# Performance work log

Measured on AMD Instinct MI355X. Metric: run time of the kernel, lower is better.

The kernel has to match this reference:

```python
import jax, jax.numpy as jnp
import numpy as np

GH, GW, H, B, IN = 4, 2, 512, 8192, 1
FC_HID = H // 2
NC = GH * GW
BN_EPS = 1e-5


def setup_inputs() -> dict:
    key = jax.random.key(0)
    ks = jax.random.split(key, 20)
    def n(k, shape, s=1.0):
        return jax.random.normal(k, shape, dtype=jnp.float32) * s
    return {
        "x": n(ks[0], (B, GH, GW)),
        "h_ext": n(ks[1], (B, H), 0.1),
        "c_ext": n(ks[2], (B, H), 0.1),
        "grid_h": n(ks[3], (GH, GW, B, H), 0.1),
        "grid_c": n(ks[4], (GH, GW, B, H), 0.1),
        "Wh": n(ks[5], (NC, H, 3 * H), (3 * H) ** -0.5),
        "bh": n(ks[6], (NC, H), 0.01),
        "Wc": n(ks[7], (NC, H, 3 * H), (3 * H) ** -0.5),
        "bc": n(ks[8], (NC, H), 0.01),
        "W_ih": n(ks[9], (NC, 4 * H, IN), 1.0),
        "W_hh": n(ks[10], (NC, 4 * H, H), H ** -0.5),
        "b_ih": n(ks[11], (NC, 4 * H), 0.01),
        "b_hh": n(ks[12], (NC, 4 * H), 0.01),
        "W1": n(ks[13], (FC_HID, 2 * H), (2 * H) ** -0.5),
        "b1": n(ks[14], (FC_HID,), 0.01),
        "W2": n(ks[15], (1, FC_HID), FC_HID ** -0.5),
        "b2": n(ks[16], (1,), 0.01),
        "gamma": jnp.ones((1,), jnp.float32),
        "beta": jnp.zeros((1,), jnp.float32),
    }


def _lattice_forward(x, h_ext, c_ext, grid_h, grid_c, Wh, bh, Wc, bc,
                     W_ih, W_hh, b_ih, b_hh, W1, b1, W2, b2, gamma, beta):
    b = x.shape[0]
    zeros = jnp.zeros((b, H), x.dtype)
    # python lists over the small fixed 4x2 grid (strict left/up dependency)
    sh = [[grid_h[i, j] for j in range(GW)] for i in range(GH)]
    sc = [[grid_c[i, j] for j in range(GW)] for i in range(GH)]
    for i in range(GH):
        for j in range(GW):
            k = i * GW + j
            h_prev, c_prev = sh[i][j], sc[i][j]
            if i == 0 and j == 0:
                h_left, c_left = h_ext, c_ext
            elif j > 0:
                h_left, c_left = sh[i][j - 1], sc[i][j - 1]
            else:
                h_left, c_left = zeros, zeros
            if i > 0:
                h_up, c_up = sh[i - 1][j], sc[i - 1][j]
            else:
                h_up, c_up = zeros, zeros
            comb_h = jnp.concatenate([h_left, h_up, h_prev], axis=1)  # [B,3H]
            comb_c = jnp.concatenate([c_left, c_up, c_prev], axis=1)
            ph = comb_h @ Wh[k].T + bh[k]  # [B,H]
            pc = comb_c @ Wc[k].T + bc[k]
            xi = x[:, i, j][:, None]  # [B,1]
            gates = xi @ W_ih[k].T + b_ih[k] + ph @ W_hh[k].T + b_hh[k]  # [B,4H]
            ig, fg, gg, og = jnp.split(gates, 4, axis=1)
            c_new = jax.nn.sigmoid(fg) * pc + jax.nn.sigmoid(ig) * jnp.tanh(gg)
            h_new = jax.nn.sigmoid(og) * jnp.tanh(c_new)
            sh[i][j], sc[i][j] = h_new, c_new
    final_h = sh[-1][-1] + h_ext
    final_c = sc[-1][-1] + c_ext
    final = jnp.concatenate([final_h, final_c], axis=1)  # [B,2H]
    hid = jax.nn.relu(final @ W1.T + b1)
    out = hid @ W2.T + b2  # [B,1]
    # BatchNorm1d in training mode: biased batch stats over the batch dim
    mu = jnp.mean(out, axis=0, keepdims=True)
    var = jnp.mean((out - mu) ** 2, axis=0, keepdims=True)
    out = gamma * (out - mu) * jax.lax.rsqrt(var + BN_EPS) + beta
    out = jax.nn.sigmoid(out)
    new_gh = jnp.stack([jnp.stack(row) for row in sh])  # [GH,GW,B,H]
    new_gc = jnp.stack([jnp.stack(row) for row in sc])
    return out, final_h, final_c, new_gh, new_gc


def reference(x, h_ext, c_ext, grid_h, grid_c, Wh, bh, Wc, bc,
              W_ih, W_hh, b_ih, b_hh, W1, b1, W2, b2, gamma, beta):
    return _lattice_forward(x, h_ext, c_ext, grid_h, grid_c, Wh, bh, Wc, bc,
                            W_ih, W_hh, b_ih, b_hh, W1, b1, W2, b2, gamma, beta)
```

## Files before the change

### kernel.cpp

```cpp
#include <hip/hip_runtime.h>
#include <stdint.h>

#define B_SZ 8192
#define H_SZ 512
static const size_t BH = (size_t)B_SZ * H_SZ;

typedef short bfrag8 __attribute__((ext_vector_type(8)));
typedef float f32x4 __attribute__((ext_vector_type(4)));

__device__ __forceinline__ unsigned short f2bf(float f) {
  union { float f; uint32_t u; } c; c.f = f;
  uint32_t u = c.u;
  uint32_t r = (u + 0x7FFFu + ((u >> 16) & 1u)) >> 16;
  return (unsigned short)r;
}
__device__ __forceinline__ float bf2f(unsigned short u) {
  union { uint32_t u; float f; } c; c.u = ((uint32_t)u) << 16;
  return c.f;
}
__device__ __forceinline__ float sigm(float x) { return 1.0f / (1.0f + __expf(-x)); }
__device__ __forceinline__ float tanh_fast(float x) {
  float cx = fminf(fmaxf(x, -15.0f), 15.0f);
  float e = __expf(2.0f * cx);
  return (e - 1.0f) / (e + 1.0f);
}

__device__ __forceinline__ void gload16(const void* g, void* l) {
  __builtin_amdgcn_global_load_lds(
      (const __attribute__((address_space(1))) void*)g,
      (__attribute__((address_space(3))) void*)l, 16, 0, 0);
}

__device__ __forceinline__ void xcd_swizzle(int& bx, int& by, int& bz) {
  int nx = gridDim.x, ny = gridDim.y, nz = gridDim.z;
  int nwg = nx * ny * nz;
  int id = blockIdx.x + nx * (blockIdx.y + ny * blockIdx.z);
  int q = nwg >> 3, r = nwg & 7;
  int xcd = id & 7, lin = id >> 3;
  int swz = (xcd < r ? xcd * (q + 1) : r * (q + 1) + (xcd - r) * q) + lin;
  bx = swz % nx; swz /= nx;
  by = swz % ny; bz = swz / ny;
}

struct PJob {
  const unsigned short* A[3];
  int co[3];
  int nseg, relu;
  const unsigned short* B;
  const float* bias;
  unsigned short* outBf;
  float* outF;
};
struct PArgs {
  PJob j[8];
  int ldA, ldB, outStride;
};

__global__ __launch_bounds__(256, 4) void pgemm_k(PArgs pa) {
  __shared__ __align__(16) char As[16384];
  __shared__ __align__(16) char Bs[16384];
  int bx, by, bz;
  xcd_swizzle(bx, by, bz);
  const PJob jb = pa.j[bz];
  const int tid = threadIdx.x;
  const int lane = tid & 63;
  const int wv = tid >> 6;
  const int wr = wv >> 1, wc = wv & 1;
  const int m0 = by * 128;

  int rowA[4], cg[4];
  const char* browPtr[4];
#pragma unroll
  for (int q = 0; q < 4; ++q) {
    int cl = q * 256 + tid;
    int row = cl >> 3, cs = cl & 7;
    cg[q] = cs ^ (row & 7);
    rowA[q] = row;
    browPtr[q] = (const char*)jb.B + (size_t)(bx * 128 + row) * pa.ldB * 2;
  }

  f32x4 acc[4][4];
#pragma unroll
  for (int a = 0; a < 4; ++a)
#pragma unroll
    for (int b = 0; b < 4; ++b) acc[a][b] = f32x4{0.f, 0.f, 0.f, 0.f};

  for (int s = 0; s < jb.nseg; ++s) {
    const char* Abase = (const char*)jb.A[s];
    const int coB = jb.co[s] * 2;
    for (int k0 = 0; k0 < 512; k0 += 64) {
#pragma unroll
      for (int q = 0; q < 4; ++q)
        gload16(Abase + ((size_t)(m0 + rowA[q]) * pa.ldA + k0) * 2 + cg[q] * 16,
                As + (q * 256 + tid) * 16);
#pragma unroll
      for (int q = 0; q < 4; ++q)
        gload16(browPtr[q] + coB + k0 * 2 + cg[q] * 16,
                Bs + (q * 256 + tid) * 16);
      __syncthreads();
#pragma unroll
      for (int ks = 0; ks < 2; ++ks) {
        bfrag8 af[4], bfr[4];
#pragma unroll
        for (int mf = 0; mf < 4; ++mf) {
          int row = wr * 64 + mf * 16 + (lane & 15);
          af[mf] = *(const bfrag8*)(As + row * 128 +
                                    ((ks * 4 + (lane >> 4)) ^ (row & 7)) * 16);
        }
#pragma unroll
        for (int nf = 0; nf < 4; ++nf) {
          int row = wc * 64 + nf * 16 + (lane & 15);
          bfr[nf] = *(const bfrag8*)(Bs + row * 128 +
                                     ((ks * 4 + (lane >> 4)) ^ (row & 7)) * 16);
        }
#pragma unroll
        for (int mf = 0; mf < 4; ++mf)
#pragma unroll
          for (int nf = 0; nf < 4; ++nf)
            acc[mf][nf] = __builtin_amdgcn_mfma_f32_16x16x32_bf16(
                af[mf], bfr[nf], acc[mf][nf], 0, 0, 0);
      }
      __syncthreads();
    }
  }

  const int c4 = lane & 15;
  const int r4 = lane >> 4;
  const int n0 = bx * 128;
#pragma unroll
  for (int nf = 0; nf < 4; ++nf) {
    int colg = n0 + wc * 64 + nf * 16 + c4;
    float bv = jb.bias[colg];
#pragma unroll
    for (int mf = 0; mf < 4; ++mf)
#pragma unroll
      for (int r = 0; r < 4; ++r) {
        int rowg = m0 + wr * 64 + mf * 16 + r4 * 4 + r;
        size_t o = (size_t)rowg * pa.outStride + colg;
        float v = acc[mf][nf][r] + bv;
        if (jb.relu) v = fmaxf(v, 0.0f);
        if (jb.outBf) jb.outBf[o] = f2bf(v);
        if (jb.outF) jb.outF[o] = v;
      }
  }
}

struct GJob {
  const unsigned short* ph;
  const unsigned short* Whh;
  const float* pc;
  float* gh; float* gc;
  unsigned short* nh; unsigned short* nc;
  int cell, last;
};
struct GArgs {
  GJob j[2];
  const float* x;
  const float* W_ih; const float* b_ih; const float* b_hh;
  const float* h_ext; const float* c_ext;
  float* fh; float* fc;
  unsigned short* finalB;
};

__global__ __launch_bounds__(256, 3) void gates_k(GArgs ga) {
  __shared__ __align__(16) char As[16384];
  __shared__ __align__(16) char Bs[16384];
  int bx, by, bz;
  xcd_swizzle(bx, by, bz);
  const GJob jb = ga.j[bz];
  const int tid = threadIdx.x;
  const int lane = tid & 63;
  const int wv = tid >> 6;
  const int wr = wv >> 1, wc = wv & 1;
  const int m0 = by * 128;

  int rowA[4], cg[4];
  const char* browPtr[4];
#pragma unroll
  for (int q = 0; q < 4; ++q) {
    int cl = q * 256 + tid;
    int row = cl >> 3, cs = cl & 7;
    cg[q] = cs ^ (row & 7);
    rowA[q] = row;
    int gate = (row >> 4) & 3;
    int hh = bx * 32 + ((row >> 6) << 4) + (row & 15);
    browPtr[q] = (const char*)jb.Whh + (size_t)(gate * 512 + hh) * 512 * 2;
  }

  f32x4 acc[4][4];
#pragma unroll
  for (int a = 0; a < 4; ++a)
#pragma unroll
    for (int b = 0; b < 4; ++b) acc[a][b] = f32x4{0.f, 0.f, 0.f, 0.f};

  for (int k0 = 0; k0 < 512; k0 += 64) {
#pragma unroll
    for (int q = 0; q < 4; ++q)
      gload16((const char*)jb.ph + ((size_t)(m0 + rowA[q]) * 512 + k0) * 2 + cg[q] * 16,
              As + (q * 256 + tid) * 16);
#pragma unroll
    for (int q = 0; q < 4; ++q)
      gload16(browPtr[q] + k0 * 2 + cg[q] * 16, Bs + (q * 256 + tid) * 16);
    __syncthreads();
#pragma unroll
    for (int ks = 0; ks < 2; ++ks) {
      bfrag8 af[4], bfr[4];
#pragma unroll
      for (int mf = 0; mf < 4; ++mf) {
        int row = wr * 64 + mf * 16 + (lane & 15);
        af[mf] = *(const bfrag8*)(As + row * 128 +
                                  ((ks * 4 + (lane >> 4)) ^ (row & 7)) * 16);
      }
#pragma unroll
      for (int nf = 0; nf < 4; ++nf) {
        int row = wc * 64 + nf * 16 + (lane & 15);
        bfr[nf] = *(const bfrag8*)(Bs + row * 128 +
                                   ((ks * 4 + (lane >> 4)) ^ (row & 7)) * 16);
      }
#pragma unroll
      for (int mf = 0; mf < 4; ++mf)
#pragma unroll
        for (int nf = 0; nf < 4; ++nf)
          acc[mf][nf] = __builtin_amdgcn_mfma_f32_16x16x32_bf16(
              af[mf], bfr[nf], acc[mf][nf], 0, 0, 0);
    }
    __syncthreads();
  }

  const int c4 = lane & 15;
  const int r4 = lane >> 4;
  int hcol = bx * 32 + wc * 16 + c4;
  const float* Wih = ga.W_ih + jb.cell * 2048;
  const float* bih = ga.b_ih + jb.cell * 2048;
  const float* bhh = ga.b_hh + jb.cell * 2048;
  float wih[4], gb[4];
#pragma unroll
  for (int q = 0; q < 4; ++q) {
    wih[q] = Wih[q * 512 + hcol];
    gb[q] = bih[q * 512 + hcol] + bhh[q * 512 + hcol];
  }
#pragma unroll
  for (int mf = 0; mf < 4; ++mf)
#pragma unroll
    for (int r = 0; r < 4; ++r) {
      int b = m0 + wr * 64 + mf * 16 + r4 * 4 + r;
      float xi = ga.x[b * 8 + jb.cell];
      float vi = acc[mf][0][r] + xi * wih[0] + gb[0];
      float vf = acc[mf][1][r] + xi * wih[1] + gb[1];
      float vg = acc[mf][2][r] + xi * wih[2] + gb[2];
      float vo = acc[mf][3][r] + xi * wih[3] + gb[3];
      size_t o = (size_t)b * 512 + hcol;
      float pcv = jb.pc[o];
      float cn = sigm(vf) * pcv + sigm(vi) * tanh_fast(vg);
      float hn = sigm(vo) * tanh_fast(cn);
      jb.gh[o] = hn;
      jb.gc[o] = cn;
      jb.nh[o] = f2bf(hn);
      jb.nc[o] = f2bf(cn);
      if (jb.last) {
        float fh = hn + ga.h_ext[o];
        float fc = cn + ga.c_ext[o];
        ga.fh[o] = fh;
        ga.fc[o] = fc;
        ga.finalB[(size_t)b * 1024 + hcol] = f2bf(fh);
        ga.finalB[(size_t)b * 1024 + 512 + hcol] = f2bf(fc);
      }
    }
}

struct CvtArgs {
  const float4* s[8];
  uint2* d[8];
  long start[9];
};
__global__ __launch_bounds__(256) void convert_many(CvtArgs ca) {
  long total = ca.start[8];
  long stride = (long)gridDim.x * blockDim.x;
  for (long idx = (long)blockIdx.x * blockDim.x + threadIdx.x; idx < total;
       idx += stride) {
    int jb = 0;
#pragma unroll
    for (int q = 1; q < 8; ++q) jb += (idx >= ca.start[q]) ? 1 : 0;
    long local = idx - ca.start[jb];
    float4 v = ca.s[jb][local];
    uint2 o;
    o.x = (uint32_t)f2bf(v.x) | ((uint32_t)f2bf(v.y) << 16);
    o.y = (uint32_t)f2bf(v.z) | ((uint32_t)f2bf(v.w) << 16);
    ca.d[jb][local] = o;
  }
}

__global__ __launch_bounds__(256)
void fc2_kernel(const unsigned short* hid, const float* W2, const float* b2,
                float* outlin) {
  int row = blockIdx.x * 4 + (threadIdx.x >> 6);
  int lane = threadIdx.x & 63;
  uint2 hv = ((const uint2*)(hid + (size_t)row * 256))[lane];
  float4 wv = ((const float4*)W2)[lane];
  float s = bf2f((unsigned short)(hv.x & 0xffffu)) * wv.x +
            bf2f((unsigned short)(hv.x >> 16)) * wv.y +
            bf2f((unsigned short)(hv.y & 0xffffu)) * wv.z +
            bf2f((unsigned short)(hv.y >> 16)) * wv.w;
#pragma unroll
  for (int o = 32; o > 0; o >>= 1) s += __shfl_down(s, o);
  if (lane == 0) outlin[row] = s + b2[0];
}

__global__ __launch_bounds__(1024)
void bn_kernel(const float* outlin, const float* gamma, const float* beta,
               float* out) {
  __shared__ float sred[16], sred2[16];
  __shared__ float smu, srs;
  float s = 0.f, s2 = 0.f;
  for (int i = threadIdx.x; i < 8192; i += 1024) {
    float v = outlin[i];
    s += v; s2 += v * v;
  }
#pragma unroll
  for (int o = 32; o > 0; o >>= 1) { s += __shfl_down(s, o); s2 += __shfl_down(s2, o); }
  if ((threadIdx.x & 63) == 0) { sred[threadIdx.x >> 6] = s; sred2[threadIdx.x >> 6] = s2; }
  __syncthreads();
  if (threadIdx.x == 0) {
    float S = 0.f, S2 = 0.f;
    for (int q = 0; q < 16; ++q) { S += sred[q]; S2 += sred2[q]; }
    float mu = S * (1.0f / 8192.0f);
    float var = S2 * (1.0f / 8192.0f) - mu * mu;
    smu = mu; srs = rsqrtf(var + 1e-5f);
  }
  __syncthreads();
  float gm = gamma[0], bt = beta[0];
  for (int i = threadIdx.x; i < 8192; i += 1024) {
    float v = (outlin[i] - smu) * srs * gm + bt;
    out[i] = sigm(v);
  }
}

extern "C" void kernel_launch(void* const* d_in, const int* in_sizes, int n_in,
                              void* d_out, int out_size, void* d_ws, size_t ws_size,
                              hipStream_t stream) {
  const float* x      = (const float*)d_in[0];
  const float* h_ext  = (const float*)d_in[1];
  const float* c_ext  = (const float*)d_in[2];
  const float* grid_h = (const float*)d_in[3];
  const float* grid_c = (const float*)d_in[4];
  const float* Wh     = (const float*)d_in[5];
  const float* bh     = (const float*)d_in[6];
  const float* Wc     = (const float*)d_in[7];
  const float* bc     = (const float*)d_in[8];
  const float* W_ih   = (const float*)d_in[9];
  const float* W_hh   = (const float*)d_in[10];
  const float* b_ih   = (const float*)d_in[11];
  const float* b_hh   = (const float*)d_in[12];
  const float* W1     = (const float*)d_in[13];
  const float* b1     = (const float*)d_in[14];
  const float* W2     = (const float*)d_in[15];
  const float* b2     = (const float*)d_in[16];
  const float* gamma  = (const float*)d_in[17];
  const float* beta   = (const float*)d_in[18];

  float* out = (float*)d_out;
  float* fh_out = out + 8192;
  float* fc_out = fh_out + BH;
  float* gh_out = fc_out + BH;
  float* gc_out = gh_out + 8 * BH;

  char* ws = (char*)d_ws;
  size_t off = 0;
  auto alloc = [&](size_t bytes) {
    char* p = ws + off;
    off = (off + bytes + 255) & ~(size_t)255;
    return p;
  };
  unsigned short* whB   = (unsigned short*)alloc(8ull * 512 * 1536 * 2);
  unsigned short* wcB   = (unsigned short*)alloc(8ull * 512 * 1536 * 2);
  unsigned short* whhB  = (unsigned short*)alloc(8ull * 2048 * 512 * 2);
  unsigned short* w1B   = (unsigned short*)alloc(256ull * 1024 * 2);
  unsigned short* hextB = (unsigned short*)alloc(BH * 2);
  unsigned short* cextB = (unsigned short*)alloc(BH * 2);
  unsigned short* prevH = (unsigned short*)alloc(8 * BH * 2);
  unsigned short* prevC = (unsigned short*)alloc(8 * BH * 2);
  unsigned short* newH  = (unsigned short*)alloc(8 * BH * 2);
  unsigned short* newC  = (unsigned short*)alloc(8 * BH * 2);
  float*          pcP   = (float*)alloc(8 * BH * 4);
  unsigned short* phB   = (unsigned short*)alloc(8 * BH * 2);
  unsigned short* finalB = (unsigned short*)alloc((size_t)B_SZ * 1024 * 2);
  unsigned short* hidB   = (unsigned short*)alloc((size_t)B_SZ * 256 * 2);
  float*          outlin = (float*)alloc((size_t)B_SZ * 4);

  {
    CvtArgs ca;
    long n4[8] = {
        8L * 512 * 1536 / 4, 8L * 512 * 1536 / 4, 8L * 2048 * 512 / 4,
        256L * 1024 / 4,     (long)BH / 4,        (long)BH / 4,
        8L * (long)BH / 4,   8L * (long)BH / 4};
    const float* srcs[8] = {Wh, Wc, W_hh, W1, h_ext, c_ext, grid_h, grid_c};
    unsigned short* dsts[8] = {whB, wcB, whhB, w1B, hextB, cextB, prevH, prevC};
    ca.start[0] = 0;
    for (int q = 0; q < 8; ++q) {
      ca.s[q] = (const float4*)srcs[q];
      ca.d[q] = (uint2*)dsts[q];
      ca.start[q + 1] = ca.start[q] + n4[q];
    }
    convert_many<<<2048, 256, 0, stream>>>(ca);
  }

  auto launch_p = [&](const int* cells, int n) {
    PArgs pa = {};
    pa.ldA = 512; pa.ldB = 1536; pa.outStride = 512;
    for (int q = 0; q < n; ++q) {
      int k = cells[q];
      int i = k >> 1, jj = k & 1;
      PJob& jh = pa.j[2 * q];
      PJob& jc = pa.j[2 * q + 1];
      jh = PJob{}; jc = PJob{};
      int ns = 0;
      if (k == 0) {
        jh.A[ns] = hextB; jc.A[ns] = cextB; jh.co[ns] = 0; jc.co[ns] = 0; ns++;
      } else if (jj > 0) {
        jh.A[ns] = newH + (size_t)(k - 1) * BH;
        jc.A[ns] = newC + (size_t)(k - 1) * BH;
        jh.co[ns] = 0; jc.co[ns] = 0; ns++;
      }
      if (i > 0) {
        jh.A[ns] = newH + (size_t)(k - 2) * BH;
        jc.A[ns] = newC + (size_t)(k - 2) * BH;
        jh.co[ns] = 512; jc.co[ns] = 512; ns++;
      }
      jh.A[ns] = prevH + (size_t)k * BH;
      jc.A[ns] = prevC + (size_t)k * BH;
      jh.co[ns] = 1024; jc.co[ns] = 1024; ns++;
      jh.nseg = ns; jc.nseg = ns;
      jh.B = whB + (size_t)k * 512 * 1536; jh.bias = bh + k * 512;
      jc.B = wcB + (size_t)k * 512 * 1536; jc.bias = bc + k * 512;
      jh.outBf = phB + (size_t)k * BH;
      jc.outF = pcP + (size_t)k * BH;
    }
    pgemm_k<<<dim3(4, 64, 2 * n), 256, 0, stream>>>(pa);
  };

  auto launch_gates = [&](const int* cells, int n) {
    GArgs ga = {};
    ga.x = x; ga.W_ih = W_ih; ga.b_ih = b_ih; ga.b_hh = b_hh;
    ga.h_ext = h_ext; ga.c_ext = c_ext;
    ga.fh = fh_out; ga.fc = fc_out; ga.finalB = finalB;
    for (int q = 0; q < n; ++q) {
      int k = cells[q];
      GJob& j = ga.j[q];
      j.ph = phB + (size_t)k * BH;
      j.Whh = whhB + (size_t)k * 2048 * 512;
      j.pc = pcP + (size_t)k * BH;
      j.gh = gh_out + (size_t)k * BH;
      j.gc = gc_out + (size_t)k * BH;
      j.nh = newH + (size_t)k * BH;
      j.nc = newC + (size_t)k * BH;
      j.cell = k; j.last = (k == 7);
    }
    gates_k<<<dim3(16, 64, n), 256, 0, stream>>>(ga);
  };

  const int diags[5][2] = {{0, -1}, {1, 2}, {3, 4}, {5, 6}, {7, -1}};
  const int dn[5] = {1, 2, 2, 2, 1};
  for (int d = 0; d < 5; ++d) {
    launch_p(diags[d], dn[d]);
    launch_gates(diags[d], dn[d]);
  }

  {
    PArgs pa = {};
    pa.ldA = 1024; pa.ldB = 1024; pa.outStride = 256;
    PJob& j = pa.j[0];
    j = PJob{};
    j.A[0] = finalB; j.co[0] = 0;
    j.A[1] = finalB + 512; j.co[1] = 512;
    j.nseg = 2; j.relu = 1;
    j.B = w1B; j.bias = b1; j.outBf = hidB;
    pgemm_k<<<dim3(2, 64, 1), 256, 0, stream>>>(pa);
  }

  fc2_kernel<<<2048, 256, 0, stream>>>(hidB, W2, b2, outlin);
  bn_kernel<<<1, 1024, 0, stream>>>(outlin, gamma, beta, out);
}
```

Baseline: 757.6 us.

## Double-buffer LDS tiles in GEMM kernels and store pc intermediate as bf16

Both the projection GEMM and the gates GEMM now stage the next K-tile into a second LDS buffer while computing on the current one. Raw barriers and vmcnt waits replace __syncthreads, and s_setprio raises wave priority during the MFMA phase. The goal is to overlap global-to-LDS loads with matrix math. The pc intermediate is also written and read as bf16 instead of fp32, which halves that traffic but slightly lowers precision. LDS grows to 64KB per block and occupancy bounds drop to 2 blocks per CU.

```diff
diff --git a/kernel.cpp b/kernel.cpp
--- a/kernel.cpp
+++ b/kernel.cpp
@@ -49,16 +49,14 @@
   const unsigned short* B;
   const float* bias;
   unsigned short* outBf;
-  float* outF;
 };
 struct PArgs {
   PJob j[8];
   int ldA, ldB, outStride;
 };
 
-__global__ __launch_bounds__(256, 4) void pgemm_k(PArgs pa) {
-  __shared__ __align__(16) char As[16384];
-  __shared__ __align__(16) char Bs[16384];
+__global__ __launch_bounds__(256, 2) void pgemm_k(PArgs pa) {
+  __shared__ __align__(16) char lds[65536];
   int bx, by, bz;
   xcd_swizzle(bx, by, bz);
   const PJob jb = pa.j[bz];
@@ -67,6 +65,7 @@
   const int wv = tid >> 6;
   const int wr = wv >> 1, wc = wv & 1;
   const int m0 = by * 128;
+  const int ldA = pa.ldA;
 
   int rowA[4], cg[4];
   const char* browPtr[4];
@@ -85,43 +84,64 @@
 #pragma unroll
     for (int b = 0; b < 4; ++b) acc[a][b] = f32x4{0.f, 0.f, 0.f, 0.f};
 
-  for (int s = 0; s < jb.nseg; ++s) {
+  const int nt = jb.nseg * 8;
+
+  auto stagef = [&](int t, int buf) {
+    int s = t >> 3, k0 = (t & 7) << 6;
     const char* Abase = (const char*)jb.A[s];
-    const int coB = jb.co[s] * 2;
-    for (int k0 = 0; k0 < 512; k0 += 64) {
-#pragma unroll
-      for (int q = 0; q < 4; ++q)
-        gload16(Abase + ((size_t)(m0 + rowA[q]) * pa.ldA + k0) * 2 + cg[q] * 16,
-                As + (q * 256 + tid) * 16);
-#pragma unroll
-      for (int q = 0; q < 4; ++q)
-        gload16(browPtr[q] + coB + k0 * 2 + cg[q] * 16,
-                Bs + (q * 256 + tid) * 16);
-      __syncthreads();
-#pragma unroll
-      for (int ks = 0; ks < 2; ++ks) {
-        bfrag8 af[4], bfr[4];
-#pragma unroll
-        for (int mf = 0; mf < 4; ++mf) {
-          int row = wr * 64 + mf * 16 + (lane & 15);
-          af[mf] = *(const bfrag8*)(As + row * 128 +
-                                    ((ks * 4 + (lane >> 4)) ^ (row & 7)) * 16);
-        }
-#pragma unroll
-        for (int nf = 0; nf < 4; ++nf) {
-          int row = wc * 64 + nf * 16 + (lane & 15);
-          bfr[nf] = *(const bfrag8*)(Bs + row * 128 +
-                                     ((ks * 4 + (lane >> 4)) ^ (row & 7)) * 16);
-        }
-#pragma unroll
-        for (int mf = 0; mf < 4; ++mf)
-#pragma unroll
-          for (int nf = 0; nf < 4; ++nf)
-            acc[mf][nf] = __builtin_amdgcn_mfma_f32_16x16x32_bf16(
-                af[mf], bfr[nf], acc[mf][nf], 0, 0, 0);
-      }
-      __syncthreads();
-    }
+    int coB = jb.co[s] * 2;
+    char* base = lds + buf * 32768;
+#pragma unroll
+    for (int q = 0; q < 4; ++q)
+      gload16(Abase + ((size_t)(m0 + rowA[q]) * ldA + k0) * 2 + cg[q] * 16,
+              base + (q * 256 + tid) * 16);
+#pragma unroll
+    for (int q = 0; q < 4; ++q)
+      gload16(browPtr[q] + coB + k0 * 2 + cg[q] * 16,
+              base + 16384 + (q * 256 + tid) * 16);
+  };
+
+  stagef(0, 0);
+  int cur = 0;
+  for (int t = 0; t < nt; ++t) {
+    if (t + 1 < nt) {
+      stagef(t + 1, cur ^ 1);
+      asm volatile("s_waitcnt vmcnt(8)" ::: "memory");
+    } else {
+      asm volatile("s_waitcnt vmcnt(0)" ::: "memory");
+    }
+    __builtin_amdgcn_s_barrier();
+    asm volatile("" ::: "memory");
+    const char* As = lds + cur * 32768;
+    const char* Bs = As + 16384;
+    __builtin_amdgcn_s_setprio(1);
+#pragma unroll
+    for (int ks = 0; ks < 2; ++ks) {
+      bfrag8 af[4], bfr[4];
+#pragma unroll
+      for (int mf = 0; mf < 4; ++mf) {
+        int row = wr * 64 + mf * 16 + (lane & 15);
+        af[mf] = *(const bfrag8*)(As + row * 128 +
+                                  ((ks * 4 + (lane >> 4)) ^ (row & 7)) * 16);
+      }
+#pragma unroll
+      for (int nf = 0; nf < 4; ++nf) {
+        int row = wc * 64 + nf * 16 + (lane & 15);
+        bfr[nf] = *(const bfrag8*)(Bs + row * 128 +
+                                   ((ks * 4 + (lane >> 4)) ^ (row & 7)) * 16);
+      }
+#pragma unroll
+      for (int mf = 0; mf < 4; ++mf)
+#pragma unroll
+        for (int nf = 0; nf < 4; ++nf)
+          acc[mf][nf] = __builtin_amdgcn_mfma_f32_16x16x32_bf16(
+              af[mf], bfr[nf], acc[mf][nf], 0, 0, 0);
+    }
+    __builtin_amdgcn_s_setprio(0);
+    asm volatile("" ::: "memory");
+    __builtin_amdgcn_s_barrier();
+    asm volatile("" ::: "memory");
+    cur ^= 1;
   }
 
   const int c4 = lane & 15;
@@ -139,8 +159,7 @@
         size_t o = (size_t)rowg * pa.outStride + colg;
         float v = acc[mf][nf][r] + bv;
         if (jb.relu) v = fmaxf(v, 0.0f);
-        if (jb.outBf) jb.outBf[o] = f2bf(v);
-        if (jb.outF) jb.outF[o] = v;
+        jb.outBf[o] = f2bf(v);
       }
   }
 }
@@ -148,7 +167,7 @@
 struct GJob {
   const unsigned short* ph;
   const unsigned short* Whh;
-  const float* pc;
+  const unsigned short* pc;
   float* gh; float* gc;
   unsigned short* nh; unsigned short* nc;
   int cell, last;
@@ -162,9 +181,8 @@
   unsigned short* finalB;
 };
 
-__global__ __launch_bounds__(256, 3) void gates_k(GArgs ga) {
-  __shared__ __align__(16) char As[16384];
-  __shared__ __align__(16) char Bs[16384];
+__global__ __launch_bounds__(256, 2) void gates_k(GArgs ga) {
+  __shared__ __align__(16) char lds[65536];
   int bx, by, bz;
   xcd_swizzle(bx, by, bz);
   const GJob jb = ga.j[bz];
@@ -193,15 +211,33 @@
 #pragma unroll
     for (int b = 0; b < 4; ++b) acc[a][b] = f32x4{0.f, 0.f, 0.f, 0.f};
 
-  for (int k0 = 0; k0 < 512; k0 += 64) {
+  auto stagef = [&](int t, int buf) {
+    int k0 = t << 6;
+    char* base = lds + buf * 32768;
 #pragma unroll
     for (int q = 0; q < 4; ++q)
       gload16((const char*)jb.ph + ((size_t)(m0 + rowA[q]) * 512 + k0) * 2 + cg[q] * 16,
-              As + (q * 256 + tid) * 16);
+              base + (q * 256 + tid) * 16);
 #pragma unroll
     for (int q = 0; q < 4; ++q)
-      gload16(browPtr[q] + k0 * 2 + cg[q] * 16, Bs + (q * 256 + tid) * 16);
-    __syncthreads();
+      gload16(browPtr[q] + k0 * 2 + cg[q] * 16,
+              base + 16384 + (q * 256 + tid) * 16);
+  };
+
+  stagef(0, 0);
+  int cur = 0;
+  for (int t = 0; t < 8; ++t) {
+    if (t + 1 < 8) {
+      stagef(t + 1, cur ^ 1);
+      asm volatile("s_waitcnt vmcnt(8)" ::: "memory");
+    } else {
+      asm volatile("s_waitcnt vmcnt(0)" ::: "memory");
+    }
+    __builtin_amdgcn_s_barrier();
+    asm volatile("" ::: "memory");
+    const char* As = lds + cur * 32768;
+    const char* Bs = As + 16384;
+    __builtin_amdgcn_s_setprio(1);
 #pragma unroll
     for (int ks = 0; ks < 2; ++ks) {
       bfrag8 af[4], bfr[4];
@@ -224,7 +260,11 @@
           acc[mf][nf] = __builtin_amdgcn_mfma_f32_16x16x32_bf16(
               af[mf], bfr[nf], acc[mf][nf], 0, 0, 0);
     }
-    __syncthreads();
+    __builtin_amdgcn_s_setprio(0);
+    asm volatile("" ::: "memory");
+    __builtin_amdgcn_s_barrier();
+    asm volatile("" ::: "memory");
+    cur ^= 1;
   }
 
   const int c4 = lane & 15;
@@ -250,7 +290,7 @@
       float vg = acc[mf][2][r] + xi * wih[2] + gb[2];
       float vo = acc[mf][3][r] + xi * wih[3] + gb[3];
       size_t o = (size_t)b * 512 + hcol;
-      float pcv = jb.pc[o];
+      float pcv = bf2f(jb.pc[o]);
       float cn = sigm(vf) * pcv + sigm(vi) * tanh_fast(vg);
       float hn = sigm(vo) * tanh_fast(cn);
       jb.gh[o] = hn;
@@ -381,7 +421,7 @@
   unsigned short* prevC = (unsigned short*)alloc(8 * BH * 2);
   unsigned short* newH  = (unsigned short*)alloc(8 * BH * 2);
   unsigned short* newC  = (unsigned short*)alloc(8 * BH * 2);
-  float*          pcP   = (float*)alloc(8 * BH * 4);
+  unsigned short* pcB   = (unsigned short*)alloc(8 * BH * 2);
   unsigned short* phB   = (unsigned short*)alloc(8 * BH * 2);
   unsigned short* finalB = (unsigned short*)alloc((size_t)B_SZ * 1024 * 2);
   unsigned short* hidB   = (unsigned short*)alloc((size_t)B_SZ * 256 * 2);
@@ -433,7 +473,7 @@
       jh.B = whB + (size_t)k * 512 * 1536; jh.bias = bh + k * 512;
       jc.B = wcB + (size_t)k * 512 * 1536; jc.bias = bc + k * 512;
       jh.outBf = phB + (size_t)k * BH;
-      jc.outF = pcP + (size_t)k * BH;
+      jc.outBf = pcB + (size_t)k * BH;
     }
     pgemm_k<<<dim3(4, 64, 2 * n), 256, 0, stream>>>(pa);
   };
@@ -448,7 +488,7 @@
       GJob& j = ga.j[q];
       j.ph = phB + (size_t)k * BH;
       j.Whh = whhB + (size_t)k * 2048 * 512;
-      j.pc = pcP + (size_t)k * BH;
+      j.pc = pcB + (size_t)k * BH;
       j.gh = gh_out + (size_t)k * BH;
       j.gc = gc_out + (size_t)k * BH;
       j.nh = newH + (size_t)k * BH;
```

After: 751.2 us. Within noise of the previous version (-0.8%).

## Replace projection and gate GEMMs with 256x256 double-buffered pipelined MFMA kernel

Applied to the files above, without the earlier changes.

Adds a templated kernel that handles both the per-cell projection GEMMs and the LSTM gate GEMMs. It uses 256x256 tiles with 512 threads, double-buffered LDS (128KB dynamic) and interleaved global-to-LDS staging with barriers and setprio around MFMA quadrants, so loads overlap compute and each tile gets more reuse. The cell projection pc is now stored as bf16 instead of fp32, halving that intermediate's traffic at some precision cost. Grids shrink a lot, which may leave CUs idle on the single-cell diagonals.

```diff
diff --git a/kernel.cpp b/kernel.cpp
--- a/kernel.cpp
+++ b/kernel.cpp
@@ -2,8 +2,7 @@
 #include <stdint.h>
 
 #define B_SZ 8192
-#define H_SZ 512
-static const size_t BH = (size_t)B_SZ * H_SZ;
+static const size_t BH = (size_t)B_SZ * 512;
 
 typedef short bfrag8 __attribute__((ext_vector_type(8)));
 typedef float f32x4 __attribute__((ext_vector_type(4)));
@@ -42,6 +41,219 @@
   by = swz % ny; bz = swz / ny;
 }
 
+struct J8 {
+  const unsigned short* A[3];
+  int co[3];
+  int nseg, relu;
+  const unsigned short* B;
+  const float* bias;
+  unsigned short* outBf;
+  const unsigned short* pc;
+  float* gh; float* gc;
+  unsigned short* nh; unsigned short* nc;
+  int cell, last;
+};
+struct A8 {
+  J8 j[4];
+  int ldA, ldB, outStride;
+  const float* x;
+  const float* W_ih; const float* b_ih; const float* b_hh;
+  const float* h_ext; const float* c_ext;
+  float* fh; float* fc;
+  unsigned short* finalB;
+};
+
+template <int MA, int NB>
+__device__ __forceinline__ void mfmaQ(f32x4 acc[8][4], const bfrag8 afr[4][2],
+                                      const bfrag8 bfr[2][2]) {
+#pragma unroll
+  for (int mfq = 0; mfq < 4; ++mfq)
+#pragma unroll
+    for (int nfq = 0; nfq < 2; ++nfq)
+#pragma unroll
+      for (int ks = 0; ks < 2; ++ks)
+        acc[MA * 4 + mfq][NB * 2 + nfq] = __builtin_amdgcn_mfma_f32_16x16x32_bf16(
+            afr[mfq][ks], bfr[nfq][ks], acc[MA * 4 + mfq][NB * 2 + nfq], 0, 0, 0);
+}
+
+#define BAR() __builtin_amdgcn_s_barrier()
+#define PRIO(x) __builtin_amdgcn_s_setprio(x)
+#define VMCNT4() asm volatile("s_waitcnt vmcnt(4)" ::: "memory")
+#define VMCNT0() asm volatile("s_waitcnt vmcnt(0)" ::: "memory")
+
+template <int MODE>
+__global__ __launch_bounds__(512, 2) void g8_k(A8 pa) {
+  extern __shared__ char lds[];
+  int bx, by, bz;
+  xcd_swizzle(bx, by, bz);
+  const J8 jb = pa.j[bz];
+  const int tid = threadIdx.x;
+  const int lane = tid & 63;
+  const int wv = tid >> 6;
+  const int wr = wv >> 2, wc = wv & 3;
+  const int m0 = by * 256;
+  const int ldA = pa.ldA;
+
+  int rowS[4], cgS[4];
+  const char* bPtr[4];
+#pragma unroll
+  for (int q = 0; q < 4; ++q) {
+    int cl = q * 512 + tid;
+    int row = cl >> 3, cs = cl & 7;
+    cgS[q] = cs ^ (row & 7);
+    rowS[q] = row;
+    int browG;
+    if (MODE == 1)
+      browG = ((row >> 4) & 3) * 512 + bx * 64 + ((row >> 6) << 4) + (row & 15);
+    else
+      browG = bx * 256 + row;
+    bPtr[q] = (const char*)jb.B + (size_t)browG * pa.ldB * 2;
+  }
+
+  auto stageA = [&](int kt, int half) {
+    int d = kt & 1, seg = kt >> 3, k0 = (kt & 7) << 6;
+    const char* Ab = (const char*)jb.A[seg];
+#pragma unroll
+    for (int q = 2 * half; q < 2 * half + 2; ++q)
+      gload16(Ab + ((size_t)(m0 + rowS[q]) * ldA + k0) * 2 + cgS[q] * 16,
+              lds + d * 32768 + (q * 512 + tid) * 16);
+  };
+  auto stageB = [&](int kt, int half) {
+    int d = kt & 1, seg = kt >> 3, k0 = (kt & 7) << 6;
+    int coB = (jb.co[seg] + k0) * 2;
+#pragma unroll
+    for (int q = 2 * half; q < 2 * half + 2; ++q)
+      gload16(bPtr[q] + coB + cgS[q] * 16,
+              lds + 65536 + d * 32768 + (q * 512 + tid) * 16);
+  };
+
+  bfrag8 afr[4][2], bfr0[2][2], bfr1[2][2];
+  auto dsA = [&](int buf, int mA) {
+    const char* base = lds + buf * 32768;
+#pragma unroll
+    for (int mfq = 0; mfq < 4; ++mfq)
+#pragma unroll
+      for (int ks = 0; ks < 2; ++ks) {
+        int row = wr * 128 + (mA * 4 + mfq) * 16 + (lane & 15);
+        afr[mfq][ks] = *(const bfrag8*)(base + row * 128 +
+                                        (((ks * 4 + (lane >> 4)) ^ (row & 7)) * 16));
+      }
+  };
+  auto dsB = [&](int buf, int nB, bfrag8 b[2][2]) {
+    const char* base = lds + 65536 + buf * 32768;
+#pragma unroll
+    for (int nfq = 0; nfq < 2; ++nfq)
+#pragma unroll
+      for (int ks = 0; ks < 2; ++ks) {
+        int row = wc * 64 + (nB * 2 + nfq) * 16 + (lane & 15);
+        b[nfq][ks] = *(const bfrag8*)(base + row * 128 +
+                                      (((ks * 4 + (lane >> 4)) ^ (row & 7)) * 16));
+      }
+  };
+
+  f32x4 acc[8][4];
+#pragma unroll
+  for (int a = 0; a < 8; ++a)
+#pragma unroll
+    for (int b = 0; b < 4; ++b) acc[a][b] = f32x4{0.f, 0.f, 0.f, 0.f};
+
+  const int nt = jb.nseg * 8;
+  const int niter = nt >> 1;
+
+  stageB(0, 0); stageB(0, 1); stageA(0, 0); stageA(0, 1); stageB(1, 0); stageB(1, 1);
+  VMCNT4();
+  BAR();
+
+  for (int i = 0; i < niter; ++i) {
+    const int kt = 2 * i;
+    const bool lastI = (i == niter - 1);
+    dsA(0, 0);
+    dsB(0, 0, bfr0);
+    stageA(kt + 1, 0);
+    BAR(); PRIO(1); mfmaQ<0, 0>(acc, afr, bfr0); PRIO(0); BAR();
+    dsB(0, 1, bfr1);
+    stageA(kt + 1, 1);
+    BAR(); PRIO(1); mfmaQ<0, 1>(acc, afr, bfr1); PRIO(0); BAR();
+    dsA(0, 1);
+    if (!lastI) stageB(kt + 2, 0);
+    BAR(); PRIO(1); mfmaQ<1, 1>(acc, afr, bfr1); PRIO(0); BAR();
+    if (!lastI) { stageB(kt + 2, 1); VMCNT4(); }
+    else        { VMCNT0(); }
+    BAR(); PRIO(1); mfmaQ<1, 0>(acc, afr, bfr0); PRIO(0); BAR();
+    dsA(1, 0);
+    dsB(1, 0, bfr0);
+    if (!lastI) stageA(kt + 2, 0);
+    BAR(); PRIO(1); mfmaQ<0, 0>(acc, afr, bfr0); PRIO(0); BAR();
+    dsB(1, 1, bfr1);
+    if (!lastI) stageA(kt + 2, 1);
+    BAR(); PRIO(1); mfmaQ<0, 1>(acc, afr, bfr1); PRIO(0); BAR();
+    dsA(1, 1);
+    if (!lastI) stageB(kt + 3, 0);
+    BAR(); PRIO(1); mfmaQ<1, 1>(acc, afr, bfr1); PRIO(0); BAR();
+    if (!lastI) { stageB(kt + 3, 1); VMCNT4(); }
+    BAR(); PRIO(1); mfmaQ<1, 0>(acc, afr, bfr0); PRIO(0); BAR();
+  }
+
+  const int c4 = lane & 15;
+  const int r4 = lane >> 4;
+  if (MODE == 0) {
+    const int n0 = bx * 256;
+#pragma unroll
+    for (int nf = 0; nf < 4; ++nf) {
+      int colg = n0 + wc * 64 + nf * 16 + c4;
+      float bv = jb.bias[colg];
+#pragma unroll
+      for (int mf = 0; mf < 8; ++mf)
+#pragma unroll
+        for (int r = 0; r < 4; ++r) {
+          int rowg = m0 + wr * 128 + mf * 16 + r4 * 4 + r;
+          size_t o = (size_t)rowg * pa.outStride + colg;
+          float v = acc[mf][nf][r] + bv;
+          if (jb.relu) v = fmaxf(v, 0.0f);
+          jb.outBf[o] = f2bf(v);
+        }
+    }
+  } else {
+    int hcol = bx * 64 + wc * 16 + c4;
+    const float* Wih = pa.W_ih + jb.cell * 2048;
+    const float* bih = pa.b_ih + jb.cell * 2048;
+    const float* bhh = pa.b_hh + jb.cell * 2048;
+    float wih[4], gb[4];
+#pragma unroll
+    for (int q = 0; q < 4; ++q) {
+      wih[q] = Wih[q * 512 + hcol];
+      gb[q] = bih[q * 512 + hcol] + bhh[q * 512 + hcol];
+    }
+#pragma unroll
+    for (int mf = 0; mf < 8; ++mf)
+#pragma unroll
+      for (int r = 0; r < 4; ++r) {
+        int b = m0 + wr * 128 + mf * 16 + r4 * 4 + r;
+        float xi = pa.x[b * 8 + jb.cell];
+        float vi = acc[mf][0][r] + xi * wih[0] + gb[0];
+        float vf = acc[mf][1][r] + xi * wih[1] + gb[1];
+        float vg = acc[mf][2][r] + xi * wih[2] + gb[2];
+        float vo = acc[mf][3][r] + xi * wih[3] + gb[3];
+        size_t o = (size_t)b * 512 + hcol;
+        float pcv = bf2f(jb.pc[o]);
+        float cn = sigm(vf) * pcv + sigm(vi) * tanh_fast(vg);
+        float hn = sigm(vo) * tanh_fast(cn);
+        jb.gh[o] = hn;
+        jb.gc[o] = cn;
+        jb.nh[o] = f2bf(hn);
+        jb.nc[o] = f2bf(cn);
+        if (jb.last) {
+          float fh = hn + pa.h_ext[o];
+          float fc = cn + pa.c_ext[o];
+          pa.fh[o] = fh;
+          pa.fc[o] = fc;
+          pa.finalB[(size_t)b * 1024 + hcol] = f2bf(fh);
+          pa.finalB[(size_t)b * 1024 + 512 + hcol] = f2bf(fc);
+        }
+      }
+  }
+}
+
 struct PJob {
   const unsigned short* A[3];
   int co[3];
@@ -49,7 +261,6 @@
   const unsigned short* B;
   const float* bias;
   unsigned short* outBf;
-  float* outF;
 };
 struct PArgs {
   PJob j[8];
@@ -139,133 +350,9 @@
         size_t o = (size_t)rowg * pa.outStride + colg;
         float v = acc[mf][nf][r] + bv;
         if (jb.relu) v = fmaxf(v, 0.0f);
-        if (jb.outBf) jb.outBf[o] = f2bf(v);
-        if (jb.outF) jb.outF[o] = v;
-      }
-  }
-}
-
-struct GJob {
-  const unsigned short* ph;
-  const unsigned short* Whh;
-  const float* pc;
-  float* gh; float* gc;
-  unsigned short* nh; unsigned short* nc;
-  int cell, last;
-};
-struct GArgs {
-  GJob j[2];
-  const float* x;
-  const float* W_ih; const float* b_ih; const float* b_hh;
-  const float* h_ext; const float* c_ext;
-  float* fh; float* fc;
-  unsigned short* finalB;
-};
-
-__global__ __launch_bounds__(256, 3) void gates_k(GArgs ga) {
-  __shared__ __align__(16) char As[16384];
-  __shared__ __align__(16) char Bs[16384];
-  int bx, by, bz;
-  xcd_swizzle(bx, by, bz);
-  const GJob jb = ga.j[bz];
-  const int tid = threadIdx.x;
-  const int lane = tid & 63;
-  const int wv = tid >> 6;
-  const int wr = wv >> 1, wc = wv & 1;
-  const int m0 = by * 128;
-
-  int rowA[4], cg[4];
-  const char* browPtr[4];
-#pragma unroll
-  for (int q = 0; q < 4; ++q) {
-    int cl = q * 256 + tid;
-    int row = cl >> 3, cs = cl & 7;
-    cg[q] = cs ^ (row & 7);
-    rowA[q] = row;
-    int gate = (row >> 4) & 3;
-    int hh = bx * 32 + ((row >> 6) << 4) + (row & 15);
-    browPtr[q] = (const char*)jb.Whh + (size_t)(gate * 512 + hh) * 512 * 2;
-  }
-
-  f32x4 acc[4][4];
-#pragma unroll
-  for (int a = 0; a < 4; ++a)
-#pragma unroll
-    for (int b = 0; b < 4; ++b) acc[a][b] = f32x4{0.f, 0.f, 0.f, 0.f};
-
-  for (int k0 = 0; k0 < 512; k0 += 64) {
-#pragma unroll
-    for (int q = 0; q < 4; ++q)
-      gload16((const char*)jb.ph + ((size_t)(m0 + rowA[q]) * 512 + k0) * 2 + cg[q] * 16,
-              As + (q * 256 + tid) * 16);
-#pragma unroll
-    for (int q = 0; q < 4; ++q)
-      gload16(browPtr[q] + k0 * 2 + cg[q] * 16, Bs + (q * 256 + tid) * 16);
-    __syncthreads();
-#pragma unroll
-    for (int ks = 0; ks < 2; ++ks) {
-      bfrag8 af[4], bfr[4];
-#pragma unroll
-      for (int mf = 0; mf < 4; ++mf) {
-        int row = wr * 64 + mf * 16 + (lane & 15);
-        af[mf] = *(const bfrag8*)(As + row * 128 +
-                                  ((ks * 4 + (lane >> 4)) ^ (row & 7)) * 16);
-      }
-#pragma unroll
-      for (int nf = 0; nf < 4; ++nf) {
-        int row = wc * 64 + nf * 16 + (lane & 15);
-        bfr[nf] = *(const bfrag8*)(Bs + row * 128 +
-                                   ((ks * 4 + (lane >> 4)) ^ (row & 7)) * 16);
-      }
-#pragma unroll
-      for (int mf = 0; mf < 4; ++mf)
-#pragma unroll
-        for (int nf = 0; nf < 4; ++nf)
-          acc[mf][nf] = __builtin_amdgcn_mfma_f32_16x16x32_bf16(
-              af[mf], bfr[nf], acc[mf][nf], 0, 0, 0);
-    }
-    __syncthreads();
-  }
-
-  const int c4 = lane & 15;
-  const int r4 = lane >> 4;
-  int hcol = bx * 32 + wc * 16 + c4;
-  const float* Wih = ga.W_ih + jb.cell * 2048;
-  const float* bih = ga.b_ih + jb.cell * 2048;
-  const float* bhh = ga.b_hh + jb.cell * 2048;
-  float wih[4], gb[4];
-#pragma unroll
-  for (int q = 0; q < 4; ++q) {
-    wih[q] = Wih[q * 512 + hcol];
-    gb[q] = bih[q * 512 + hcol] + bhh[q * 512 + hcol];
-  }
-#pragma unroll
-  for (int mf = 0; mf < 4; ++mf)
-#pragma unroll
-    for (int r = 0; r < 4; ++r) {
-      int b = m0 + wr * 64 + mf * 16 + r4 * 4 + r;
-      float xi = ga.x[b * 8 + jb.cell];
-      float vi = acc[mf][0][r] + xi * wih[0] + gb[0];
-      float vf = acc[mf][1][r] + xi * wih[1] + gb[1];
-      float vg = acc[mf][2][r] + xi * wih[2] + gb[2];
-      float vo = acc[mf][3][r] + xi * wih[3] + gb[3];
-      size_t o = (size_t)b * 512 + hcol;
-      float pcv = jb.pc[o];
-      float cn = sigm(vf) * pcv + sigm(vi) * tanh_fast(vg);
-      float hn = sigm(vo) * tanh_fast(cn);
-      jb.gh[o] = hn;
-      jb.gc[o] = cn;
-      jb.nh[o] = f2bf(hn);
-      jb.nc[o] = f2bf(cn);
-      if (jb.last) {
-        float fh = hn + ga.h_ext[o];
-        float fc = cn + ga.c_ext[o];
-        ga.fh[o] = fh;
-        ga.fc[o] = fc;
-        ga.finalB[(size_t)b * 1024 + hcol] = f2bf(fh);
-        ga.finalB[(size_t)b * 1024 + 512 + hcol] = f2bf(fc);
-      }
-    }
+        jb.outBf[o] = f2bf(v);
+      }
+  }
 }
 
 struct CvtArgs {
@@ -381,11 +468,16 @@
   unsigned short* prevC = (unsigned short*)alloc(8 * BH * 2);
   unsigned short* newH  = (unsigned short*)alloc(8 * BH * 2);
   unsigned short* newC  = (unsigned short*)alloc(8 * BH * 2);
-  float*          pcP   = (float*)alloc(8 * BH * 4);
+  unsigned short* pcB   = (unsigned short*)alloc(8 * BH * 2);
   unsigned short* phB   = (unsigned short*)alloc(8 * BH * 2);
   unsigned short* finalB = (unsigned short*)alloc((size_t)B_SZ * 1024 * 2);
   unsigned short* hidB   = (unsigned short*)alloc((size_t)B_SZ * 256 * 2);
   float*          outlin = (float*)alloc((size_t)B_SZ * 4);
+
+  hipFuncSetAttribute((const void*)g8_k<0>,
+                      hipFuncAttributeMaxDynamicSharedMemorySize, 131072);
+  hipFuncSetAttribute((const void*)g8_k<1>,
+                      hipFuncAttributeMaxDynamicSharedMemorySize, 131072);
 
   {
     CvtArgs ca;
@@ -405,14 +497,14 @@
   }
 
   auto launch_p = [&](const int* cells, int n) {
-    PArgs pa = {};
+    A8 pa = {};
     pa.ldA = 512; pa.ldB = 1536; pa.outStride = 512;
     for (int q = 0; q < n; ++q) {
       int k = cells[q];
       int i = k >> 1, jj = k & 1;
-      PJob& jh = pa.j[2 * q];
-      PJob& jc = pa.j[2 * q + 1];
-      jh = PJob{}; jc = PJob{};
+      J8& jh = pa.j[2 * q];
+      J8& jc = pa.j[2 * q + 1];
+      jh = J8{}; jc = J8{};
       int ns = 0;
       if (k == 0) {
         jh.A[ns] = hextB; jc.A[ns] = cextB; jh.co[ns] = 0; jc.co[ns] = 0; ns++;
@@ -433,29 +525,31 @@
       jh.B = whB + (size_t)k * 512 * 1536; jh.bias = bh + k * 512;
       jc.B = wcB + (size_t)k * 512 * 1536; jc.bias = bc + k * 512;
       jh.outBf = phB + (size_t)k * BH;
-      jc.outF = pcP + (size_t)k * BH;
+      jc.outBf = pcB + (size_t)k * BH;
     }
-    pgemm_k<<<dim3(4, 64, 2 * n), 256, 0, stream>>>(pa);
+    g8_k<0><<<dim3(2, 32, 2 * n), 512, 131072, stream>>>(pa);
   };
 
   auto launch_gates = [&](const int* cells, int n) {
-    GArgs ga = {};
+    A8 ga = {};
+    ga.ldA = 512; ga.ldB = 512; ga.outStride = 512;
     ga.x = x; ga.W_ih = W_ih; ga.b_ih = b_ih; ga.b_hh = b_hh;
     ga.h_ext = h_ext; ga.c_ext = c_ext;
     ga.fh = fh_out; ga.fc = fc_out; ga.finalB = finalB;
     for (int q = 0; q < n; ++q) {
       int k = cells[q];
-      GJob& j = ga.j[q];
-      j.ph = phB + (size_t)k * BH;
-      j.Whh = whhB + (size_t)k * 2048 * 512;
-      j.pc = pcP + (size_t)k * BH;
+      J8& j = ga.j[q];
+      j = J8{};
+      j.A[0] = phB + (size_t)k * BH; j.co[0] = 0; j.nseg = 1;
+      j.B = whhB + (size_t)k * 2048 * 512;
+      j.pc = pcB + (size_t)k * BH;
       j.gh = gh_out + (size_t)k * BH;
       j.gc = gc_out + (size_t)k * BH;
       j.nh = newH + (size_t)k * BH;
       j.nc = newC + (size_t)k * BH;
       j.cell = k; j.last = (k == 7);
     }
-    gates_k<<<dim3(16, 64, n), 256, 0, stream>>>(ga);
+    g8_k<1><<<dim3(8, 32, n), 512, 131072, stream>>>(ga);
   };
 
   const int diags[5][2] = {{0, -1}, {1, 2}, {3, 4}, {5, 6}, {7, -1}};
```

Result: slower. 876.9 us, median of 3 (+15.8%).
